# Optimization experiments

Hardware: AMD Instinct MI355X
Metric: run time of the kernel (lower is better)

Reference implementation:

```python
import jax, jax.numpy as jnp
import numpy as np

N = 50000      # nodes
E = 800000     # edges
D_IN, D_HID, D_OUT = 1433, 64, 7
EPS = 1e-7       # eps[float32] in hgcn Hyperboloid
MIN_NORM = 1e-15
MAX_NORM = 1e6
# c = 1 -> K = 1/c = 1, sqrtK = 1 (folded into constants below)


def proj(x):
    # reset time coordinate so point lies on the hyperboloid
    y = x[:, 1:]
    y_sqnorm = jnp.sum(y * y, axis=1, keepdims=True)
    x0 = jnp.sqrt(jnp.clip(1.0 + y_sqnorm, EPS))
    return jnp.concatenate([x0, y], axis=1)


def proj_tan0(u):
    return jnp.concatenate([jnp.zeros_like(u[:, :1]), u[:, 1:]], axis=1)


def expmap0(u):
    x = u[:, 1:]
    x_norm = jnp.clip(jnp.linalg.norm(x, axis=1, keepdims=True), MIN_NORM)
    theta = x_norm
    res = jnp.concatenate([jnp.cosh(theta), jnp.sinh(theta) * x / x_norm], axis=1)
    return proj(res)


def logmap0(x):
    y = x[:, 1:]
    y_norm = jnp.clip(jnp.linalg.norm(y, axis=1, keepdims=True), MIN_NORM)
    theta = jnp.clip(x[:, :1], 1.0 + EPS)
    return jnp.concatenate([jnp.zeros_like(theta), jnp.arccosh(theta) * y / y_norm], axis=1)


def minkowski_dot(x, y):
    return jnp.sum(x * y, axis=-1, keepdims=True) - 2.0 * x[:, :1] * y[:, :1]


def proj_tan(u, x):
    ux = jnp.sum(x[:, 1:] * u[:, 1:], axis=1, keepdims=True)
    v0 = ux / jnp.clip(x[:, :1], EPS)
    return jnp.concatenate([v0, u[:, 1:]], axis=1)


def expmap(u, x):
    normu = jnp.sqrt(jnp.clip(minkowski_dot(u, u), EPS))
    normu = jnp.minimum(normu, MAX_NORM)
    theta = jnp.clip(normu, MIN_NORM)
    result = jnp.cosh(theta) * x + jnp.sinh(theta) * u / theta
    return proj(result)


def ptransp0(x, u):
    x0, y = x[:, :1], x[:, 1:]
    y_norm = jnp.clip(jnp.linalg.norm(y, axis=1, keepdims=True), MIN_NORM)
    yn = y / y_norm
    v = jnp.concatenate([-y_norm, (1.0 - x0) * yn], axis=1)
    alpha = jnp.sum(yn * u[:, 1:], axis=1, keepdims=True)
    return proj_tan(u - alpha * v, x)


def mobius_add(x, y):
    u = logmap0(y)
    v = ptransp0(x, u)
    return expmap(v, x)


def hyp_linear(x, W, b):
    # mobius_matvec then hyperbolic bias add (dropout=0)
    mv = expmap0(logmap0(x) @ W.T)
    res = proj(mv)
    hyp_bias = proj(expmap0(proj_tan0(b[None, :])))
    return proj(mobius_add(res, hyp_bias))


def hyp_agg(x, row, col, edge_weight):
    # spmm(adj, logmap0(x)) via edge-list scatter-add
    xt = logmap0(x)
    msg = edge_weight[:, None] * xt[col]          # [E, d]
    support = jax.ops.segment_sum(msg, row, num_segments=N)
    return proj(expmap0(support))


def hyp_act(x):
    xt = jax.nn.relu(logmap0(x))
    xt = proj_tan0(xt)
    return proj(expmap0(xt))


def setup_inputs() -> dict:
    key = jax.random.key(0)
    ks = jax.random.split(key, 8)
    return {
        "x": jax.random.normal(ks[0], (N, D_IN), dtype=jnp.float32),
        "row": jax.random.randint(ks[1], (E,), 0, N),
        "col": jax.random.randint(ks[2], (E,), 0, N),
        "edge_weight": jax.random.uniform(ks[3], (E,), dtype=jnp.float32) * 0.1,
        "W1": jax.random.normal(ks[4], (D_HID, D_IN), dtype=jnp.float32) * 0.02,
        "b1": jax.random.normal(ks[5], (D_HID,), dtype=jnp.float32) * 0.02,
        "W2": jax.random.normal(ks[6], (D_OUT, D_HID), dtype=jnp.float32) * 0.05,
        "b2": jax.random.normal(ks[7], (D_OUT,), dtype=jnp.float32) * 0.02,
    }


def reference(x, row, col, edge_weight, W1, b1, W2, b2):
    # map features to the hyperboloid
    x_hyp = proj(expmap0(proj_tan0(x)))
    # layer 1: HypLinear -> HypAgg -> HypAct
    h = hyp_act(hyp_agg(hyp_linear(x_hyp, W1, b1), row, col, edge_weight))
    # layer 2
    h = hyp_act(hyp_agg(hyp_linear(h, W2, b2), row, col, edge_weight))
    # back to tangent space at origin
    return proj_tan0(logmap0(h))
```

## Files before the change

kernel.cpp:

```cpp
#include <hip/hip_runtime.h>
#include <hip/hip_bf16.h>

#define NN 50000
#define EE 800000
#define DIN 1433
#define KTOT 1432
#define KHALF 716
#define NKT 23
#define NB 196
#define EPSC 1e-7f
#define MINN 1e-15f
#define MAXN 1e6f

typedef __attribute__((ext_vector_type(8))) short bf16x8;
typedef __attribute__((ext_vector_type(4))) float f32x4;

#define WF_OFF     0
#define Z1A_OFF    94208
#define Z1B_OFF    (Z1A_OFF + 3200000)
#define XTB_OFF    (Z1B_OFF + 3200000)
#define XT3_OFF    (XTB_OFF + 1600000)
#define CNT_OFF    (XT3_OFF + 400000)
#define ROWPTR_OFF (CNT_OFF + 50000)
#define CUR_OFF    (ROWPTR_OFF + 50002)
#define BSUM_OFF   (CUR_OFF + 50000)
#define BOFF_OFF   (BSUM_OFF + 256)
#define UB_OFF     (BOFF_OFF + 256)
#define EP_OFF     (UB_OFF + 128)

__device__ __forceinline__ float wsum(float v) {
#pragma unroll
  for (int o = 1; o < 64; o <<= 1) v += __shfl_xor(v, o, 64);
  return v;
}

__device__ __forceinline__ float gsum8(float v) {
#pragma unroll
  for (int o = 1; o < 8; o <<= 1) v += __shfl_xor(v, o, 64);
  return v;
}

__device__ __forceinline__ void split_bf(float v, unsigned int& hbits16, unsigned int& lbits16) {
  unsigned int b = __float_as_uint(v);
  unsigned int hb = b & 0xFFFF0000u;
  float r = v - __uint_as_float(hb);
  unsigned int lb = __float_as_uint(r);
  lbits16 = (lb + 0x7FFFu + ((lb >> 16) & 1u)) >> 16;
  hbits16 = hb >> 16;
}

__device__ __forceinline__ unsigned short f2bf_rne(float v) {
  unsigned int b = __float_as_uint(v);
  return (unsigned short)((b + 0x7FFFu + ((b >> 16) & 1u)) >> 16);
}
__device__ __forceinline__ float bf2f(unsigned short u) {
  return __uint_as_float(((unsigned int)u) << 16);
}

__device__ __forceinline__ float fsinh(float x) {
  float e = __expf(x);
  return 0.5f * (e - __fdividef(1.f, e));
}
__device__ __forceinline__ float facoshp(float z) {
  return __logf(z + sqrtf(fmaxf(z * z - 1.f, 0.f)));
}

__device__ float bias_tangent(const float* b, int lane, int D) {
  const bool sp = (lane >= 1) && (lane < D);
  float bsp = sp ? b[lane] : 0.f;
  float rb = fmaxf(sqrtf(wsum(bsp * bsp)), MINN);
  float bsh = fsinh(rb);
  float hb = sp ? bsh * __fdividef(bsp, rb) : 0.f;
  float hbn2 = wsum(hb * hb);
  float hb0 = sqrtf(fmaxf(1.f + hbn2, EPSC));
  float hbyn = fmaxf(sqrtf(hbn2), MINN);
  return sp ? facoshp(fmaxf(hb0, 1.f + EPSC)) * __fdividef(hb, hbyn) : 0.f;
}

__device__ float chain_with_u(float z, float u, int lane, int D) {
  const bool sp = (lane >= 1) && (lane < D);
  float s = sp ? z : 0.f;
  float r = fmaxf(sqrtf(wsum(s * s)), MINN);
  float sh = fsinh(r);
  float y = sp ? sh * __fdividef(s, r) : 0.f;
  float yn2 = wsum(y * y);
  float x0 = sqrtf(fmaxf(1.f + yn2, EPSC));
  float y_norm = fmaxf(sqrtf(yn2), MINN);
  float ynv = sp ? __fdividef(y, y_norm) : 0.f;
  float alpha = wsum(ynv * u);
  float wsp = sp ? u - alpha * (1.f - x0) * ynv : 0.f;
  float ux = wsum(y * wsp);
  float v0 = __fdividef(ux, fmaxf(x0, EPSC));
  float vt = (lane == 0) ? v0 : wsp;
  float md = wsum(vt * vt) - 2.f * v0 * v0;
  float nu = sqrtf(fmaxf(md, EPSC));
  nu = fminf(nu, MAXN);
  float th = fmaxf(nu, MINN);
  float e = __expf(th), ei = __fdividef(1.f, e);
  float cth = 0.5f * (e + ei), sth = 0.5f * (e - ei);
  float resx = (lane == 0) ? x0 : y;
  float eres = fmaf(cth, resx, sth * __fdividef(vt, th));
  float en2 = wsum(sp ? eres * eres : 0.f);
  float e0 = sqrtf(fmaxf(1.f + en2, EPSC));
  float eyn = fmaxf(sqrtf(en2), MINN);
  return sp ? facoshp(fmaxf(e0, 1.f + EPSC)) * __fdividef(eres, eyn) : 0.f;
}

__device__ float agg_act_chain(float sin_, int lane, int D) {
  const bool sp = (lane >= 1) && (lane < D);
  float s = sp ? sin_ : 0.f;
  float r = fmaxf(sqrtf(wsum(s * s)), MINN);
  float sh = fsinh(r);
  float g = sp ? sh * __fdividef(s, r) : 0.f;
  float gn2 = wsum(g * g);
  float g0 = sqrtf(fmaxf(1.f + gn2, EPSC));
  float gyn = fmaxf(sqrtf(gn2), MINN);
  float l = sp ? facoshp(fmaxf(g0, 1.f + EPSC)) * __fdividef(g, gyn) : 0.f;
  float t = fmaxf(l, 0.f);
  float rt = fmaxf(sqrtf(wsum(t * t)), MINN);
  float sht = fsinh(rt);
  float h = sp ? sht * __fdividef(t, rt) : 0.f;
  float hn2 = wsum(h * h);
  float h0 = sqrtf(fmaxf(1.f + hn2, EPSC));
  float hyn = fmaxf(sqrtf(hn2), MINN);
  return sp ? facoshp(fmaxf(h0, 1.f + EPSC)) * __fdividef(h, hyn) : 0.f;
}

__device__ float agg_act_chain8(float sin_, int f) {
  const bool sp = (f >= 1) && (f < 7);
  float s = sp ? sin_ : 0.f;
  float r = fmaxf(sqrtf(gsum8(s * s)), MINN);
  float sh = fsinh(r);
  float g = sp ? sh * __fdividef(s, r) : 0.f;
  float gn2 = gsum8(g * g);
  float g0 = sqrtf(fmaxf(1.f + gn2, EPSC));
  float gyn = fmaxf(sqrtf(gn2), MINN);
  float l = sp ? facoshp(fmaxf(g0, 1.f + EPSC)) * __fdividef(g, gyn) : 0.f;
  float t = fmaxf(l, 0.f);
  float rt = fmaxf(sqrtf(gsum8(t * t)), MINN);
  float sht = fsinh(rt);
  float h = sp ? sht * __fdividef(t, rt) : 0.f;
  float hn2 = gsum8(h * h);
  float h0 = sqrtf(fmaxf(1.f + hn2, EPSC));
  float hyn = fmaxf(sqrtf(hn2), MINN);
  return sp ? facoshp(fmaxf(h0, 1.f + EPSC)) * __fdividef(h, hyn) : 0.f;
}

__global__ __launch_bounds__(256) void prep_wb_zero(const float* __restrict__ W1,
                                                    const float* __restrict__ b1,
                                                    const float* __restrict__ b2,
                                                    unsigned short* __restrict__ wfrag,
                                                    float* __restrict__ ub,
                                                    int* __restrict__ cnt) {
  if (blockIdx.x >= 93) {
    int i = (blockIdx.x - 93) * 256 + threadIdx.x;
    if (i < NN) cnt[i] = 0;
    return;
  }
  if (blockIdx.x == 92) {
    const int w = threadIdx.x >> 6, lane = threadIdx.x & 63;
    if (w == 0) ub[lane] = bias_tangent(b1, lane, 64);
    else if (w == 1) ub[64 + lane] = bias_tangent(b2, lane, 7);
    return;
  }
  int idx = blockIdx.x * 256 + threadIdx.x;
  int lane = idx & 63;
  int c = (idx >> 6) & 7;
  int rest = idx >> 9;
  int kt = rest % NKT;
  int half = rest / NKT;
  int type = c >> 2, nt = c & 3;
  int col = nt * 16 + (lane & 15);
  unsigned short vals[8];
#pragma unroll
  for (int i = 0; i < 8; ++i) {
    int lk = kt * 32 + (lane >> 4) * 8 + i;
    float wv = (lk < KHALF) ? W1[col * DIN + half * KHALF + lk + 1] : 0.f;
    unsigned int h16, l16;
    split_bf(wv, h16, l16);
    vals[i] = (unsigned short)((type == 0) ? h16 : l16);
  }
  unsigned short* dst = wfrag + (((size_t)(half * NKT + kt) * 8 + c) * 64 + lane) * 8;
#pragma unroll
  for (int i = 0; i < 8; ++i) dst[i] = vals[i];
}

__global__ __launch_bounds__(256) void k_hist(const int* __restrict__ row, int* __restrict__ cnt) {
  int e = blockIdx.x * 256 + threadIdx.x;
  if (e < EE) atomicAdd(&cnt[row[e]], 1);
}

__global__ __launch_bounds__(256) void k_blocksum(const int* __restrict__ cnt,
                                                  int* __restrict__ bsum) {
  __shared__ int wpart[4];
  int i = blockIdx.x * 256 + threadIdx.x;
  int v = (i < NN) ? cnt[i] : 0;
  int s = v;
#pragma unroll
  for (int o = 1; o < 64; o <<= 1) s += __shfl_xor(s, o, 64);
  if ((threadIdx.x & 63) == 0) wpart[threadIdx.x >> 6] = s;
  __syncthreads();
  if (threadIdx.x == 0) bsum[blockIdx.x] = wpart[0] + wpart[1] + wpart[2] + wpart[3];
}

__global__ __launch_bounds__(256) void k_scanb(const int* __restrict__ bsum,
                                               int* __restrict__ boff) {
  __shared__ int s[256];
  int t = threadIdx.x;
  int v = (t < NB) ? bsum[t] : 0;
  s[t] = v;
  __syncthreads();
  for (int o = 1; o < 256; o <<= 1) {
    int a = (t >= o) ? s[t - o] : 0;
    __syncthreads();
    s[t] += a;
    __syncthreads();
  }
  if (t < NB) boff[t] = s[t] - v;
}

__global__ __launch_bounds__(256) void k_apply(const int* __restrict__ cnt,
                                               const int* __restrict__ boff,
                                               int* __restrict__ rowptr, int* __restrict__ cur) {
  __shared__ int s[256];
  int i = blockIdx.x * 256 + threadIdx.x;
  int t = threadIdx.x;
  int v = (i < NN) ? cnt[i] : 0;
  s[t] = v;
  __syncthreads();
  for (int o = 1; o < 256; o <<= 1) {
    int a = (t >= o) ? s[t - o] : 0;
    __syncthreads();
    s[t] += a;
    __syncthreads();
  }
  int ex = s[t] - v + boff[blockIdx.x];
  if (i < NN) { rowptr[i] = ex; cur[i] = ex; }
  if (i == NN - 1) rowptr[NN] = EE;
}

__global__ __launch_bounds__(256) void k_scatter(const int* __restrict__ row,
                                                 const int* __restrict__ col,
                                                 const float* __restrict__ ew,
                                                 int* __restrict__ cur, uint2* __restrict__ ep) {
  int e = blockIdx.x * 256 + threadIdx.x;
  if (e < EE) {
    int p = atomicAdd(&cur[row[e]], 1);
    uint2 q;
    q.x = (unsigned int)col[e];
    q.y = __float_as_uint(ew[e]);
    ep[p] = q;
  }
}

__global__ __launch_bounds__(256) void gemm_half(const float* __restrict__ x,
                                                 const unsigned short* __restrict__ wfrag,
                                                 float* __restrict__ z) {
  __shared__ __align__(16) float XA[3 * 1024];
  __shared__ __align__(16) unsigned short BB[2][8][64][8];
  const int tid = threadIdx.x;
  const int w = tid >> 6, lane = tid & 63;
  const int row0 = blockIdx.x * 32;
  const int half = blockIdx.y;
  const unsigned short* wf = wfrag + (size_t)half * NKT * 4096;
  float* zp = z + (size_t)half * 3200000;
  const int nt0 = (w >> 1) * 2;

  auto stageB = [&](int kt, int p) {
    const unsigned short* src = wf + (size_t)kt * 4096 + (2 * w) * 512 + lane * 8;
    __builtin_amdgcn_global_load_lds(
        (const __attribute__((address_space(1))) unsigned int*)src,
        (__attribute__((address_space(3))) unsigned int*)(&BB[p][2 * w][0][0]), 16, 0, 0);
    __builtin_amdgcn_global_load_lds(
        (const __attribute__((address_space(1))) unsigned int*)(src + 512),
        (__attribute__((address_space(3))) unsigned int*)(&BB[p][2 * w + 1][0][0]), 16, 0, 0);
  };
  auto stageA = [&](int kt, int q) {
    const int r = w * 8 + (lane >> 3);
    const int lb = (lane & 7) ^ (r & 7);
    int grow = row0 + r; if (grow >= NN) grow = NN - 1;
    size_t off = (size_t)grow * DIN + 1 + half * KHALF + kt * 32 + lb * 4;
    if (off > (size_t)NN * DIN - 4) off = (size_t)NN * DIN - 4;
    __builtin_amdgcn_global_load_lds(
        (const __attribute__((address_space(1))) unsigned int*)(x + off),
        (__attribute__((address_space(3))) unsigned int*)(XA + q * 1024 + w * 256),
        16, 0, 0);
  };

  f32x4 acc[2];
  acc[0] = (f32x4){0.f, 0.f, 0.f, 0.f};
  acc[1] = (f32x4){0.f, 0.f, 0.f, 0.f};

  stageB(0, 0);
  stageA(0, 0);
  stageA(1, 1);
  __builtin_amdgcn_sched_barrier(0);
  asm volatile("s_waitcnt vmcnt(1)" ::: "memory");
  __builtin_amdgcn_s_barrier();
  __builtin_amdgcn_sched_barrier(0);

  const int rr = (w & 1) * 16 + (lane & 15);
  const int b0 = (lane >> 4) * 2;
  const int pb0 = (b0 ^ (rr & 7)) * 4;
  const int pb1 = ((b0 + 1) ^ (rr & 7)) * 4;

  for (int kt = 0; kt < NKT; ++kt) {
    if (kt + 1 < NKT) stageB(kt + 1, (kt + 1) & 1);
    if (kt + 2 < NKT) stageA(kt + 2, (kt + 2) % 3);
    const float* xa = XA + (kt % 3) * 1024 + rr * 32;
    float4 f0 = *(const float4*)(xa + pb0);
    float4 f1 = *(const float4*)(xa + pb1);
    float af[8] = {f0.x, f0.y, f0.z, f0.w, f1.x, f1.y, f1.z, f1.w};
    unsigned int h[8], l[8];
#pragma unroll
    for (int j = 0; j < 8; ++j) split_bf(af[j], h[j], l[j]);
    bf16x8 ah, al;
#pragma unroll
    for (int j = 0; j < 8; ++j) { ah[j] = (short)h[j]; al[j] = (short)l[j]; }
    bf16x8 bh[2], bl[2];
#pragma unroll
    for (int n = 0; n < 2; ++n) {
      bh[n] = *(const bf16x8*)&BB[kt & 1][nt0 + n][lane][0];
      bl[n] = *(const bf16x8*)&BB[kt & 1][4 + nt0 + n][lane][0];
    }
    __builtin_amdgcn_s_setprio(1);
#pragma unroll
    for (int n = 0; n < 2; ++n) {
      acc[n] = __builtin_amdgcn_mfma_f32_16x16x32_bf16(ah, bh[n], acc[n], 0, 0, 0);
      acc[n] = __builtin_amdgcn_mfma_f32_16x16x32_bf16(ah, bl[n], acc[n], 0, 0, 0);
      acc[n] = __builtin_amdgcn_mfma_f32_16x16x32_bf16(al, bh[n], acc[n], 0, 0, 0);
    }
    __builtin_amdgcn_s_setprio(0);
    if (kt + 1 < NKT) {
      __builtin_amdgcn_sched_barrier(0);
      asm volatile("s_waitcnt lgkmcnt(0)" ::: "memory");
      if (kt + 2 < NKT) asm volatile("s_waitcnt vmcnt(1)" ::: "memory");
      else              asm volatile("s_waitcnt vmcnt(0)" ::: "memory");
      __builtin_amdgcn_s_barrier();
      __builtin_amdgcn_sched_barrier(0);
    }
  }
#pragma unroll
  for (int n = 0; n < 2; ++n)
#pragma unroll
    for (int i = 0; i < 4; ++i) {
      int orow = row0 + (w & 1) * 16 + (lane >> 4) * 4 + i;
      int ocol = (nt0 + n) * 16 + (lane & 15);
      if (orow < NN) zp[(size_t)orow * 64 + ocol] = acc[n][i];
    }
}

__global__ __launch_bounds__(256) void node1(const float* __restrict__ z1a,
                                             const float* __restrict__ z1b,
                                             const float* __restrict__ ub,
                                             unsigned short* __restrict__ xtb) {
  const int node = blockIdx.x * 4 + (threadIdx.x >> 6);
  const int lane = threadIdx.x & 63;
  const int idx = node * 64 + lane;
  float z = z1a[idx] + z1b[idx];
  float u1 = ub[lane];
  float o = chain_with_u(z, u1, lane, 64);
  xtb[idx] = f2bf_rne(o);
}

__global__ __launch_bounds__(256) void agg1_node2(const int* __restrict__ rowptr,
                                                  const uint2* __restrict__ ep,
                                                  const unsigned short* __restrict__ xtb,
                                                  const float* __restrict__ W2,
                                                  const float* __restrict__ ub,
                                                  float* __restrict__ xt3) {
  const int node = blockIdx.x * 4 + (threadIdx.x >> 6);
  const int lane = threadIdx.x & 63;
  const int s0 = rowptr[node], s1 = rowptr[node + 1];
  float a0 = 0.f, a1 = 0.f, a2 = 0.f, a3 = 0.f;
  float a4 = 0.f, a5 = 0.f, a6 = 0.f, a7 = 0.f;
  int p = s0;
  for (; p + 8 <= s1; p += 8) {
    uint2 q0 = ep[p], q1 = ep[p + 1], q2 = ep[p + 2], q3 = ep[p + 3];
    uint2 q4 = ep[p + 4], q5 = ep[p + 5], q6 = ep[p + 6], q7 = ep[p + 7];
    a0 = fmaf(__uint_as_float(q0.y), bf2f(xtb[(size_t)q0.x * 64 + lane]), a0);
    a1 = fmaf(__uint_as_float(q1.y), bf2f(xtb[(size_t)q1.x * 64 + lane]), a1);
    a2 = fmaf(__uint_as_float(q2.y), bf2f(xtb[(size_t)q2.x * 64 + lane]), a2);
    a3 = fmaf(__uint_as_float(q3.y), bf2f(xtb[(size_t)q3.x * 64 + lane]), a3);
    a4 = fmaf(__uint_as_float(q4.y), bf2f(xtb[(size_t)q4.x * 64 + lane]), a4);
    a5 = fmaf(__uint_as_float(q5.y), bf2f(xtb[(size_t)q5.x * 64 + lane]), a5);
    a6 = fmaf(__uint_as_float(q6.y), bf2f(xtb[(size_t)q6.x * 64 + lane]), a6);
    a7 = fmaf(__uint_as_float(q7.y), bf2f(xtb[(size_t)q7.x * 64 + lane]), a7);
  }
  for (; p < s1; ++p) {
    uint2 q = ep[p];
    a0 = fmaf(__uint_as_float(q.y), bf2f(xtb[(size_t)q.x * 64 + lane]), a0);
  }
  float acc = ((a0 + a1) + (a2 + a3)) + ((a4 + a5) + (a6 + a7));
  float xt2 = agg_act_chain(acc, lane, 64);
  float z2 = 0.f;
#pragma unroll
  for (int jj = 1; jj < 7; ++jj) {
    float wv = W2[jj * 64 + lane];
    float sjj = wsum(xt2 * wv);
    if (lane == jj) z2 = sjj;
  }
  float u2 = ub[64 + lane];
  float o = chain_with_u(z2, u2, lane, 7);
  if (lane < 8) xt3[node * 8 + lane] = o;
}

__global__ __launch_bounds__(256) void agg2_final(const int* __restrict__ rowptr,
                                                  const uint2* __restrict__ ep,
                                                  const float* __restrict__ xt3,
                                                  float* __restrict__ out) {
  const int node = blockIdx.x * 32 + (threadIdx.x >> 3);
  const int f = threadIdx.x & 7;
  const int nc = (node < NN) ? node : (NN - 1);
  const int s0 = rowptr[nc], s1 = rowptr[nc + 1];
  float a0 = 0.f, a1 = 0.f, a2 = 0.f, a3 = 0.f;
  int p = s0;
  for (; p + 4 <= s1; p += 4) {
    uint2 q0 = ep[p], q1 = ep[p + 1], q2 = ep[p + 2], q3 = ep[p + 3];
    a0 = fmaf(__uint_as_float(q0.y), xt3[(size_t)q0.x * 8 + f], a0);
    a1 = fmaf(__uint_as_float(q1.y), xt3[(size_t)q1.x * 8 + f], a1);
    a2 = fmaf(__uint_as_float(q2.y), xt3[(size_t)q2.x * 8 + f], a2);
    a3 = fmaf(__uint_as_float(q3.y), xt3[(size_t)q3.x * 8 + f], a3);
  }
  for (; p < s1; ++p) {
    uint2 q = ep[p];
    a0 = fmaf(__uint_as_float(q.y), xt3[(size_t)q.x * 8 + f], a0);
  }
  float acc = (a0 + a1) + (a2 + a3);
  float o = agg_act_chain8(acc, f);
  if (node < NN && f < 7) out[node * 7 + f] = o;
}

extern "C" void kernel_launch(void* const* d_in, const int* in_sizes, int n_in,
                              void* d_out, int out_size, void* d_ws, size_t ws_size,
                              hipStream_t stream) {
  const float* x = (const float*)d_in[0];
  const int* row = (const int*)d_in[1];
  const int* col = (const int*)d_in[2];
  const float* ew = (const float*)d_in[3];
  const float* W1 = (const float*)d_in[4];
  const float* b1 = (const float*)d_in[5];
  const float* W2 = (const float*)d_in[6];
  const float* b2 = (const float*)d_in[7];
  float* ws = (float*)d_ws;
  unsigned short* wfrag = (unsigned short*)(ws + WF_OFF);
  float* z1a = ws + Z1A_OFF;
  float* z1b = ws + Z1B_OFF;
  unsigned short* xtb = (unsigned short*)(ws + XTB_OFF);
  float* xt3 = ws + XT3_OFF;
  int* cnt = (int*)(ws + CNT_OFF);
  int* rowptr = (int*)(ws + ROWPTR_OFF);
  int* cur = (int*)(ws + CUR_OFF);
  int* bsum = (int*)(ws + BSUM_OFF);
  int* boff = (int*)(ws + BOFF_OFF);
  float* ub = ws + UB_OFF;
  uint2* ep = (uint2*)(ws + EP_OFF);
  float* out = (float*)d_out;

  prep_wb_zero<<<dim3(289), dim3(256), 0, stream>>>(W1, b1, b2, wfrag, ub, cnt);

  k_hist<<<dim3(3125), dim3(256), 0, stream>>>(row, cnt);
  k_blocksum<<<dim3(NB), dim3(256), 0, stream>>>(cnt, bsum);
  k_scanb<<<dim3(1), dim3(256), 0, stream>>>(bsum, boff);
  k_apply<<<dim3(NB), dim3(256), 0, stream>>>(cnt, boff, rowptr, cur);
  k_scatter<<<dim3(3125), dim3(256), 0, stream>>>(row, col, ew, cur, ep);

  gemm_half<<<dim3(1563, 2), dim3(256), 0, stream>>>(x, wfrag, z1a);
  node1<<<dim3(12500), dim3(256), 0, stream>>>(z1a, z1b, ub, xtb);

  agg1_node2<<<dim3(12500), dim3(256), 0, stream>>>(rowptr, ep, xtb, W2, ub, xt3);
  agg2_final<<<dim3(1563), dim3(256), 0, stream>>>(rowptr, ep, xt3, out);
}
```

Measured before the change: 298.8 us.

## Fuse edge histogram into GEMM launch and edge scatter into node1 launch

Folds the CSR-building histogram into the GEMM kernel as an extra grid slice (blockIdx.y==2), and folds the edge scatter into the node1 kernel as extra trailing blocks. This removes two kernel launches and lets the atomic-bound graph preprocessing run alongside the dense GEMM and the per-node work. The cost is heterogeneous blocks inside one launch. The histogram blocks still declare the GEMM's shared memory, which may affect how they are scheduled.

```diff
diff --git a/kernel.cpp b/kernel.cpp
--- a/kernel.cpp
+++ b/kernel.cpp
@@ -185,11 +185,6 @@
   for (int i = 0; i < 8; ++i) dst[i] = vals[i];
 }
 
-__global__ __launch_bounds__(256) void k_hist(const int* __restrict__ row, int* __restrict__ cnt) {
-  int e = blockIdx.x * 256 + threadIdx.x;
-  if (e < EE) atomicAdd(&cnt[row[e]], 1);
-}
-
 __global__ __launch_bounds__(256) void k_blocksum(const int* __restrict__ cnt,
                                                   int* __restrict__ bsum) {
   __shared__ int wpart[4];
@@ -239,23 +234,18 @@
   if (i == NN - 1) rowptr[NN] = EE;
 }
 
-__global__ __launch_bounds__(256) void k_scatter(const int* __restrict__ row,
-                                                 const int* __restrict__ col,
-                                                 const float* __restrict__ ew,
-                                                 int* __restrict__ cur, uint2* __restrict__ ep) {
-  int e = blockIdx.x * 256 + threadIdx.x;
-  if (e < EE) {
-    int p = atomicAdd(&cur[row[e]], 1);
-    uint2 q;
-    q.x = (unsigned int)col[e];
-    q.y = __float_as_uint(ew[e]);
-    ep[p] = q;
-  }
-}
-
-__global__ __launch_bounds__(256) void gemm_half(const float* __restrict__ x,
+__global__ __launch_bounds__(256) void gemm_hist(const float* __restrict__ x,
                                                  const unsigned short* __restrict__ wfrag,
-                                                 float* __restrict__ z) {
+                                                 float* __restrict__ z,
+                                                 const int* __restrict__ row,
+                                                 int* __restrict__ cnt) {
+  if (blockIdx.y == 2) {
+    int e = blockIdx.x * 512 + threadIdx.x;
+    if (e < EE) atomicAdd(&cnt[row[e]], 1);
+    e += 256;
+    if (e < EE) atomicAdd(&cnt[row[e]], 1);
+    return;
+  }
   __shared__ __align__(16) float XA[3 * 1024];
   __shared__ __align__(16) unsigned short BB[2][8][64][8];
   const int tid = threadIdx.x;
@@ -350,10 +340,26 @@
     }
 }
 
-__global__ __launch_bounds__(256) void node1(const float* __restrict__ z1a,
-                                             const float* __restrict__ z1b,
-                                             const float* __restrict__ ub,
-                                             unsigned short* __restrict__ xtb) {
+__global__ __launch_bounds__(256) void node1_scatter(const float* __restrict__ z1a,
+                                                     const float* __restrict__ z1b,
+                                                     const float* __restrict__ ub,
+                                                     unsigned short* __restrict__ xtb,
+                                                     const int* __restrict__ row,
+                                                     const int* __restrict__ col,
+                                                     const float* __restrict__ ew,
+                                                     int* __restrict__ cur,
+                                                     uint2* __restrict__ ep) {
+  if (blockIdx.x >= 12500) {
+    int e = (blockIdx.x - 12500) * 256 + threadIdx.x;
+    if (e < EE) {
+      int p = atomicAdd(&cur[row[e]], 1);
+      uint2 q;
+      q.x = (unsigned int)col[e];
+      q.y = __float_as_uint(ew[e]);
+      ep[p] = q;
+    }
+    return;
+  }
   const int node = blockIdx.x * 4 + (threadIdx.x >> 6);
   const int lane = threadIdx.x & 63;
   const int idx = node * 64 + lane;
@@ -459,14 +465,14 @@
 
   prep_wb_zero<<<dim3(289), dim3(256), 0, stream>>>(W1, b1, b2, wfrag, ub, cnt);
 
-  k_hist<<<dim3(3125), dim3(256), 0, stream>>>(row, cnt);
+  gemm_hist<<<dim3(1563, 3), dim3(256), 0, stream>>>(x, wfrag, z1a, row, cnt);
+
   k_blocksum<<<dim3(NB), dim3(256), 0, stream>>>(cnt, bsum);
   k_scanb<<<dim3(1), dim3(256), 0, stream>>>(bsum, boff);
   k_apply<<<dim3(NB), dim3(256), 0, stream>>>(cnt, boff, rowptr, cur);
-  k_scatter<<<dim3(3125), dim3(256), 0, stream>>>(row, col, ew, cur, ep);
-
-  gemm_half<<<dim3(1563, 2), dim3(256), 0, stream>>>(x, wfrag, z1a);
-  node1<<<dim3(12500), dim3(256), 0, stream>>>(z1a, z1b, ub, xtb);
+
+  node1_scatter<<<dim3(15625), dim3(256), 0, stream>>>(z1a, z1b, ub, xtb,
+                                                       row, col, ew, cur, ep);
 
   agg1_node2<<<dim3(12500), dim3(256), 0, stream>>>(rowptr, ep, xtb, W2, ub, xt3);
   agg2_final<<<dim3(1563), dim3(256), 0, stream>>>(rowptr, ep, xt3, out);
```

Result: faster. 283.8 us (-5.0%).
